# Kernel tuning notes

Hardware: AMD Instinct MI355X
Metric: run time of the kernel (lower is better)

Reference implementation:

```python
import jax, jax.numpy as jnp
import numpy as np

PAD = 3            # pad_size
K = 3              # kernel_size
MAX_DISP = 20      # max_displacement
STRIDE1 = 1
STRIDE2 = 2

B, C, H, W = 4, 128, 192, 192


def _correlation(input1, input2):
    """FlowNetC/PWC-Net correlation cost volume (correlation_pwc semantics).

    input1, input2: [B, C, H, W]
    returns: [B, D*D, Hout, Wout] where D = 2*(MAX_DISP//STRIDE2)+1.
    """
    b, c, h, w = input1.shape
    kr = (K - 1) // 2                      # kernel radius
    br = kr + MAX_DISP                     # border radius
    hp, wp = h + 2 * PAD, w + 2 * PAD      # padded sizes
    hout = (hp - 2 * br) // STRIDE1
    wout = (wp - 2 * br) // STRIDE1
    gr = MAX_DISP // STRIDE2               # neighborhood grid radius
    disp = jnp.arange(-gr, gr + 1, dtype=jnp.int32) * STRIDE2
    # channel order: tj (dy) outer, ti (dx) inner, matching the CUDA kernel
    dyx = jnp.stack(jnp.meshgrid(disp, disp, indexing='ij'), axis=-1).reshape(-1, 2)

    pad1 = jnp.pad(input1, ((0, 0), (0, 0), (PAD, PAD), (PAD, PAD)))
    pad2 = jnp.pad(input2, ((0, 0), (0, 0), (PAD, PAD), (PAD, PAD)))

    # region of pad1 touched by all outputs (stride1 == 1)
    hh, ww = hout * STRIDE1 + 2 * kr, wout * STRIDE1 + 2 * kr
    s1 = pad1[:, :, MAX_DISP:MAX_DISP + hh, MAX_DISP:MAX_DISP + ww]
    nelems = K * K * c

    def step(_, d):
        dy, dx = d[0], d[1]
        s2 = jax.lax.dynamic_slice(pad2, (0, 0, MAX_DISP + dy, MAX_DISP + dx),
                                   (b, c, hh, ww))
        prod = jnp.sum(s1 * s2, axis=1)  # [B, hh, ww] reduce channels
        summed = jax.lax.reduce_window(prod, 0.0, jax.lax.add,
                                       (1, K, K), (1, STRIDE1, STRIDE1), 'VALID')
        return None, summed / nelems      # [B, Hout, Wout]

    _, out = jax.lax.scan(step, None, dyx)   # [D*D, B, Hout, Wout]
    return jnp.transpose(out, (1, 0, 2, 3))  # [B, D*D, Hout, Wout]


def setup_inputs() -> dict:
    key = jax.random.key(0)
    k1, k2 = jax.random.split(key)
    input1 = jax.random.normal(k1, (B, C, H, W), dtype=jnp.float32)
    input2 = jax.random.normal(k2, (B, C, H, W), dtype=jnp.float32)
    return {"input1": input1, "input2": input2}


def reference(input1, input2):
    return _correlation(input1, input2)
```

## Files before the change

kernel.cpp:

```cpp
#include <hip/hip_runtime.h>
#include <hip/hip_bf16.h>


#define C_    128
#define H_    192
#define W_    192
#define HW_   36864
#define NE_   18874368
#define CORR_E 44036496
#define WS_NEED 163570464ull

typedef __attribute__((ext_vector_type(8))) short short8;
typedef __attribute__((ext_vector_type(4))) float floatx4;

__device__ __forceinline__ float bf2f(ushort h) {
    uint u = ((uint)h) << 16;
    return __builtin_bit_cast(float, u);
}
__device__ __forceinline__ ushort f2bf(float f) {
    __hip_bfloat16 hb = __float2bfloat16(f);
    return *(ushort*)&hb;
}

__global__ __launch_bounds__(256)
void cvt_t_kernel(const float* __restrict__ a, const float* __restrict__ b,
                  ushort* __restrict__ dst0) {
    __shared__ ushort tile[64 * 132];
    const float* src = blockIdx.z ? b : a;
    ushort* dst = dst0 + (size_t)blockIdx.z * NE_;
    const int bb = blockIdx.y;
    const int hw0 = blockIdx.x * 64;
    const int t = threadIdx.x;
    const int xr = (t & 15) * 4;
    const int c0 = t >> 4;
    const float* sbase = src + (size_t)bb * C_ * HW_ + hw0;
#pragma unroll
    for (int pass = 0; pass < 8; ++pass) {
        const int c = c0 + 16 * pass;
        float4 v = *(const float4*)(sbase + (size_t)c * HW_ + xr);
        tile[(xr + 0) * 132 + c] = f2bf(v.x);
        tile[(xr + 1) * 132 + c] = f2bf(v.y);
        tile[(xr + 2) * 132 + c] = f2bf(v.z);
        tile[(xr + 3) * 132 + c] = f2bf(v.w);
    }
    __syncthreads();
    ushort* obase = dst + ((size_t)bb * HW_ + hw0) * 128;
#pragma unroll
    for (int pass = 0; pass < 4; ++pass) {
        const int u = t + 256 * pass;
        const int x = u >> 4, oc = u & 15;
        short8 vv = *(const short8*)&tile[x * 132 + oc * 8];
        *(short8*)(obase + (size_t)x * 128 + oc * 8) = vv;
    }
}

__global__ __launch_bounds__(256, 6)
void corr_mfma(const ushort* __restrict__ in1t, const ushort* __restrict__ in2t,
               ushort* __restrict__ corrw) {
    __shared__ ushort ctile[2][21 * 136];
    const int tid = threadIdx.x;
    const int lin = blockIdx.x + 5 * (blockIdx.y + 20 * blockIdx.z);
    const int zz = lin & 7;
    const int rem = lin >> 3;
    const int j0 = (rem % 5) * 32;
    const int r2 = rem / 5;
    const int ytile = r2 % 20;
    const int d0 = (r2 / 20) * 7;
    const int b = zz >> 1, q = zz & 1;
    const int ybase = q + 8 * ytile;
    const int lane = tid & 63, wav = tid >> 6;
    const int yrow = wav >> 1, p = wav & 1;
    const int mn = lane & 15, quad = lane >> 4;

    const int ax = j0 + 17 + 2 * mn + p;
    short8 afr[2][4];
#pragma unroll
    for (int a = 0; a < 2; ++a) {
        const int arow = ybase + 2 * yrow + 4 * a + 17;
        const ushort* aptr = in1t + ((size_t)((b * H_ + arow) * W_ + ax)) * C_ + quad * 8;
#pragma unroll
        for (int kb = 0; kb < 4; ++kb) afr[a][kb] = *(const short8*)(aptr + kb * 32);
    }

    const int ybY = ybase + 2 * yrow - 3;
    const ushort* bptr[3];
    bool colok[3];
#pragma unroll
    for (int u3 = 0; u3 < 3; ++u3) {
        const int s = u3 * 16 + mn;
        const int xp = j0 - 3 + p + 2 * s;
        colok[u3] = ((unsigned)xp < (unsigned)W_) && (s <= 36);
        bptr[u3] = in2t + (ptrdiff_t)((b * H_ + ybY) * W_ + xp) * C_ + quad * 8;
    }

    const short8 z8 = {0, 0, 0, 0, 0, 0, 0, 0};
    const size_t planebase = (size_t)b * 441;

    for (int dyi = d0; dyi < d0 + 7; ++dyi) {
        floatx4 acc[2][3];
#pragma unroll
        for (int a = 0; a < 2; ++a)
#pragma unroll
            for (int u3 = 0; u3 < 3; ++u3) acc[a][u3] = (floatx4){0.f, 0.f, 0.f, 0.f};
#pragma unroll
        for (int a = 0; a < 2; ++a) {
            const int yb = ybY + 2 * dyi + 4 * a;
            if ((unsigned)yb < (unsigned)H_) {
                const ptrdiff_t roff = (ptrdiff_t)(2 * dyi + 4 * a) * W_ * C_;
#pragma unroll
                for (int u3 = 0; u3 < 3; ++u3) {
                    short8 b0 = z8, b1 = z8, b2 = z8, b3 = z8;
                    if (colok[u3]) {
                        const ushort* bp = bptr[u3] + roff;
                        b0 = *(const short8*)(bp);
                        b1 = *(const short8*)(bp + 32);
                        b2 = *(const short8*)(bp + 64);
                        b3 = *(const short8*)(bp + 96);
                    }
                    acc[a][u3] = __builtin_amdgcn_mfma_f32_16x16x32_bf16(afr[a][0], b0, acc[a][u3], 0, 0, 0);
                    acc[a][u3] = __builtin_amdgcn_mfma_f32_16x16x32_bf16(afr[a][1], b1, acc[a][u3], 0, 0, 0);
                    acc[a][u3] = __builtin_amdgcn_mfma_f32_16x16x32_bf16(afr[a][2], b2, acc[a][u3], 0, 0, 0);
                    acc[a][u3] = __builtin_amdgcn_mfma_f32_16x16x32_bf16(afr[a][3], b3, acc[a][u3], 0, 0, 0);
                }
            }
        }

        ushort* ct = &ctile[dyi & 1][0];
#pragma unroll
        for (int a = 0; a < 2; ++a) {
            const int rr = yrow + 2 * a;
#pragma unroll
            for (int u3 = 0; u3 < 3; ++u3) {
#pragma unroll
                for (int v = 0; v < 4; ++v) {
                    const int mr = quad * 4 + v;
                    const int t = u3 * 16 + mn - mr;
                    if (t >= 0 && t <= 20)
                        ct[t * 136 + rr * 34 + 2 * mr + p] = f2bf(acc[a][u3][v]);
                }
            }
        }
        __syncthreads();
#pragma unroll
        for (int it = 0; it < 6; ++it) {
            const int idx = tid + it * 256;
            if (idx < 1344) {
                const int t = idx >> 6, rem2 = idx & 63;
                const int rr = rem2 >> 4, x2 = (rem2 & 15) << 1;
                const uint val = *(const uint*)(ct + t * 136 + rr * 34 + x2);
                const int Y = ybase + 2 * rr, X = j0 + x2;
                if (Y < 158 && X < 158) {
                    const size_t off = ((planebase + (size_t)(dyi * 21 + t)) * 158 + Y) * 158 + X;
                    *(uint*)(corrw + off) = val;
                }
            }
        }
    }
}

__global__ __launch_bounds__(192)
void window_kernel(const ushort* __restrict__ corrw, float* __restrict__ out) {
    __shared__ uint wsl[34 * 80];
    const int tid = threadIdx.x;
    const int i0 = blockIdx.x * 32;
    const int plane = blockIdx.y;
    const ushort* cp = corrw + (size_t)plane * 24964;
    for (int task = tid; task < 2720; task += 192) {
        const int r = task / 80;
        const int dc = task - r * 80;
        const int row = i0 + r;
        if (dc < 79 && row < 158)
            wsl[task] = *(const uint*)(cp + row * 158 + dc * 2);
    }
    __syncthreads();
    if (tid < 156) {
        const ushort* cl = (const ushort*)wsl;
        const float sc = 1.f / 1152.f;
        const ushort* rp0 = cl + tid;
        float s0 = bf2f(rp0[0]) + bf2f(rp0[1]) + bf2f(rp0[2]);
        const ushort* rp1 = cl + 160 + tid;
        float s1 = bf2f(rp1[0]) + bf2f(rp1[1]) + bf2f(rp1[2]);
#pragma unroll
        for (int r = 2; r < 34; ++r) {
            const ushort* rp = cl + r * 160 + tid;
            const float s2 = bf2f(rp[0]) + bf2f(rp[1]) + bf2f(rp[2]);
            const int row = i0 + r - 2;
            if (row < 156)
                out[(size_t)plane * 24336 + (size_t)row * 156 + tid] =
                    (s0 + s1 + s2) * sc;
            s0 = s1; s1 = s2;
        }
    }
}

#define OUT_HW 156
#define NDISP 21
#define TILE_OUT 14
#define TILE_CORR 16
#define S2W 56
#define NT 256

__global__ __launch_bounds__(NT, 4)
void corr_fallback(const float* __restrict__ in1, const float* __restrict__ in2,
                   float* __restrict__ out) {
    __shared__ float s2s[TILE_CORR * S2W];
    __shared__ float corrs[NDISP * TILE_CORR * TILE_CORR];
    const int tid = threadIdx.x;
    const int tx = tid & 15;
    const int ty = tid >> 4;
    const int tj = blockIdx.x;
    const int ti = blockIdx.y;
    const int z = blockIdx.z;
    const int b = z / NDISP;
    const int dyi = z - b * NDISP;
    const int dy = 2 * dyi - 20;
    const int y0 = ti * TILE_OUT;
    const int x0 = tj * TILE_OUT;
    const int y = y0 + ty;
    const int x = x0 + tx;
    float acc[NDISP];
#pragma unroll
    for (int d = 0; d < NDISP; ++d) acc[d] = 0.f;
    const float* p1 = in1 + (size_t)b * C_ * HW_ + (size_t)(y + 17) * W_ + (x + 17);
    const float* p2base = in2 + (size_t)b * C_ * HW_;
    for (int c = 0; c < C_; ++c) {
        const float a = p1[(size_t)c * HW_];
        const float* p2 = p2base + (size_t)c * HW_;
        for (int idx = tid; idx < TILE_CORR * S2W; idx += NT) {
            const int r = idx / S2W;
            const int cc = idx - r * S2W;
            const int gr = y0 + r + 17 + dy;
            const int gc = x0 + cc - 3;
            float v = 0.f;
            if ((unsigned)gr < H_ && (unsigned)gc < W_) v = p2[gr * W_ + gc];
            s2s[idx] = v;
        }
        __syncthreads();
        const float* srow = &s2s[ty * S2W + tx];
#pragma unroll
        for (int d = 0; d < NDISP; ++d) acc[d] += a * srow[2 * d];
        __syncthreads();
    }
#pragma unroll
    for (int d = 0; d < NDISP; ++d)
        corrs[d * (TILE_CORR * TILE_CORR) + tid] = acc[d];
    __syncthreads();
    const float scale = 1.f / 1152.f;
    for (int o = tid; o < NDISP * TILE_OUT * TILE_OUT; o += NT) {
        const int d = o / (TILE_OUT * TILE_OUT);
        const int rem = o - d * (TILE_OUT * TILE_OUT);
        const int i = rem / TILE_OUT;
        const int j = rem - i * TILE_OUT;
        const float* cpt = &corrs[d * (TILE_CORR * TILE_CORR) + i * TILE_CORR + j];
        const float s = cpt[0] + cpt[1] + cpt[2]
                      + cpt[16] + cpt[17] + cpt[18]
                      + cpt[32] + cpt[33] + cpt[34];
        const int ig = y0 + i;
        const int jg = x0 + j;
        if (ig < OUT_HW && jg < OUT_HW) {
            const size_t oidx = (((size_t)b * (NDISP * NDISP) + (size_t)dyi * NDISP + d)
                                 * OUT_HW + ig) * OUT_HW + jg;
            out[oidx] = s * scale;
        }
    }
}

extern "C" void kernel_launch(void* const* d_in, const int* in_sizes, int n_in,
                              void* d_out, int out_size, void* d_ws, size_t ws_size,
                              hipStream_t stream) {
    const float* in1 = (const float*)d_in[0];
    const float* in2 = (const float*)d_in[1];
    float* out = (float*)d_out;

    if (ws_size >= WS_NEED) {
        ushort* wsp = (ushort*)d_ws;
        ushort* in1t = wsp;
        ushort* in2t = wsp + (size_t)NE_;
        ushort* corrw = wsp + (size_t)2 * NE_;
        cvt_t_kernel<<<dim3(576, 4, 2), 256, 0, stream>>>(in1, in2, wsp);
        corr_mfma<<<dim3(5, 20, 24), 256, 0, stream>>>(in1t, in2t, corrw);
        window_kernel<<<dim3(5, 1764), 192, 0, stream>>>(corrw, out);
    } else {
        corr_fallback<<<dim3(12, 12, 84), 256, 0, stream>>>(in1, in2, out);
    }
}
```

Baseline: 616.4 us.

## Prefetch next displacement row's B fragments and merge dy chunks per block

Each block now loops over all 21 vertical displacements instead of a chunk of 7, cutting the grid to a third. The A fragments are then loaded once per block rather than once per chunk. B fragments for the next displacement are software-prefetched into registers while the current MFMAs and the tile store run, so global load latency overlaps with compute. Launch bounds drop from 6 to 3 blocks per CU to make room for the extra registers, which lowers occupancy and gives fewer, longer blocks.

```diff
diff --git a/kernel.cpp b/kernel.cpp
--- a/kernel.cpp
+++ b/kernel.cpp
@@ -54,7 +54,7 @@
     }
 }
 
-__global__ __launch_bounds__(256, 6)
+__global__ __launch_bounds__(256, 3)
 void corr_mfma(const ushort* __restrict__ in1t, const ushort* __restrict__ in2t,
                ushort* __restrict__ corrw) {
     __shared__ ushort ctile[2][21 * 136];
@@ -63,9 +63,7 @@
     const int zz = lin & 7;
     const int rem = lin >> 3;
     const int j0 = (rem % 5) * 32;
-    const int r2 = rem / 5;
-    const int ytile = r2 % 20;
-    const int d0 = (r2 / 20) * 7;
+    const int ytile = rem / 5;
     const int b = zz >> 1, q = zz & 1;
     const int ybase = q + 8 * ytile;
     const int lane = tid & 63, wav = tid >> 6;
@@ -83,47 +81,59 @@
     }
 
     const int ybY = ybase + 2 * yrow - 3;
-    const ushort* bptr[3];
+    const int xp0 = j0 - 3 + p + 2 * mn;
+    const ushort* bptr0 = in2t + (ptrdiff_t)((b * H_ + ybY) * W_ + xp0) * C_ + quad * 8;
     bool colok[3];
 #pragma unroll
     for (int u3 = 0; u3 < 3; ++u3) {
         const int s = u3 * 16 + mn;
-        const int xp = j0 - 3 + p + 2 * s;
+        const int xp = xp0 + 32 * u3;
         colok[u3] = ((unsigned)xp < (unsigned)W_) && (s <= 36);
-        bptr[u3] = in2t + (ptrdiff_t)((b * H_ + ybY) * W_ + xp) * C_ + quad * 8;
     }
 
     const short8 z8 = {0, 0, 0, 0, 0, 0, 0, 0};
     const size_t planebase = (size_t)b * 441;
 
-    for (int dyi = d0; dyi < d0 + 7; ++dyi) {
-        floatx4 acc[2][3];
-#pragma unroll
-        for (int a = 0; a < 2; ++a)
-#pragma unroll
-            for (int u3 = 0; u3 < 3; ++u3) acc[a][u3] = (floatx4){0.f, 0.f, 0.f, 0.f};
+    short8 bfr[2][3][4];
+    auto loadB = [&](int dyi) {
 #pragma unroll
         for (int a = 0; a < 2; ++a) {
             const int yb = ybY + 2 * dyi + 4 * a;
-            if ((unsigned)yb < (unsigned)H_) {
-                const ptrdiff_t roff = (ptrdiff_t)(2 * dyi + 4 * a) * W_ * C_;
-#pragma unroll
-                for (int u3 = 0; u3 < 3; ++u3) {
-                    short8 b0 = z8, b1 = z8, b2 = z8, b3 = z8;
-                    if (colok[u3]) {
-                        const ushort* bp = bptr[u3] + roff;
-                        b0 = *(const short8*)(bp);
-                        b1 = *(const short8*)(bp + 32);
-                        b2 = *(const short8*)(bp + 64);
-                        b3 = *(const short8*)(bp + 96);
-                    }
-                    acc[a][u3] = __builtin_amdgcn_mfma_f32_16x16x32_bf16(afr[a][0], b0, acc[a][u3], 0, 0, 0);
-                    acc[a][u3] = __builtin_amdgcn_mfma_f32_16x16x32_bf16(afr[a][1], b1, acc[a][u3], 0, 0, 0);
-                    acc[a][u3] = __builtin_amdgcn_mfma_f32_16x16x32_bf16(afr[a][2], b2, acc[a][u3], 0, 0, 0);
-                    acc[a][u3] = __builtin_amdgcn_mfma_f32_16x16x32_bf16(afr[a][3], b3, acc[a][u3], 0, 0, 0);
+            const bool rok = ((unsigned)yb < (unsigned)H_);
+            const ptrdiff_t roff = (ptrdiff_t)(2 * dyi + 4 * a) * (W_ * C_);
+#pragma unroll
+            for (int u3 = 0; u3 < 3; ++u3) {
+                if (rok && colok[u3]) {
+                    const ushort* bp = bptr0 + roff + u3 * (32 * C_);
+                    bfr[a][u3][0] = *(const short8*)(bp);
+                    bfr[a][u3][1] = *(const short8*)(bp + 32);
+                    bfr[a][u3][2] = *(const short8*)(bp + 64);
+                    bfr[a][u3][3] = *(const short8*)(bp + 96);
+                } else {
+                    bfr[a][u3][0] = z8; bfr[a][u3][1] = z8;
+                    bfr[a][u3][2] = z8; bfr[a][u3][3] = z8;
                 }
             }
         }
+    };
+
+    loadB(0);
+    for (int dyi = 0; dyi < 21; ++dyi) {
+        floatx4 acc[2][3];
+#pragma unroll
+        for (int a = 0; a < 2; ++a)
+#pragma unroll
+            for (int u3 = 0; u3 < 3; ++u3) acc[a][u3] = (floatx4){0.f, 0.f, 0.f, 0.f};
+#pragma unroll
+        for (int a = 0; a < 2; ++a)
+#pragma unroll
+            for (int u3 = 0; u3 < 3; ++u3) {
+                acc[a][u3] = __builtin_amdgcn_mfma_f32_16x16x32_bf16(afr[a][0], bfr[a][u3][0], acc[a][u3], 0, 0, 0);
+                acc[a][u3] = __builtin_amdgcn_mfma_f32_16x16x32_bf16(afr[a][1], bfr[a][u3][1], acc[a][u3], 0, 0, 0);
+                acc[a][u3] = __builtin_amdgcn_mfma_f32_16x16x32_bf16(afr[a][2], bfr[a][u3][2], acc[a][u3], 0, 0, 0);
+                acc[a][u3] = __builtin_amdgcn_mfma_f32_16x16x32_bf16(afr[a][3], bfr[a][u3][3], acc[a][u3], 0, 0, 0);
+            }
+        if (dyi < 20) loadB(dyi + 1);
 
         ushort* ct = &ctile[dyi & 1][0];
 #pragma unroll
@@ -278,7 +288,7 @@
         ushort* in2t = wsp + (size_t)NE_;
         ushort* corrw = wsp + (size_t)2 * NE_;
         cvt_t_kernel<<<dim3(576, 4, 2), 256, 0, stream>>>(in1, in2, wsp);
-        corr_mfma<<<dim3(5, 20, 24), 256, 0, stream>>>(in1t, in2t, corrw);
+        corr_mfma<<<dim3(5, 20, 8), 256, 0, stream>>>(in1t, in2t, corrw);
         window_kernel<<<dim3(5, 1764), 192, 0, stream>>>(corrw, out);
     } else {
         corr_fallback<<<dim3(12, 12, 84), 256, 0, stream>>>(in1, in2, out);
```

Result: slower. 703.5 us (+14.1%).
